# Kernel optimization log

Hardware: AMD Instinct MI355X
Metric: run time of the kernel (lower is better)

The kernel has to match this reference:

```python
import jax, jax.numpy as jnp
import numpy as np

LN_EPS = 1e-3  # keras LayerNormalization default epsilon


def _prefix_weights(S, dtype):
    # W[i, j] = 1/(i-j)^2 for j < i, else 0  (distance = i - j)
    idx = jnp.arange(S)
    diff = idx[:, None] - idx[None, :]
    safe = jnp.where(diff > 0, diff, 1).astype(dtype)
    return jnp.where(diff > 0, 1.0 / (safe * safe), jnp.zeros((), dtype))


def setup_inputs() -> dict:
    key = jax.random.key(0)
    k1, k2 = jax.random.split(key)
    B, S, E = 2, 512, 256
    x = jax.random.normal(k1, (B, S, E), dtype=jnp.float32)
    concept_map = jax.random.normal(k2, (E, E, E), dtype=jnp.float32) * 0.02
    gamma = jnp.ones((E,), dtype=jnp.float32)
    beta = jnp.zeros((E,), dtype=jnp.float32)
    return {"x": x, "concept_map": concept_map, "gamma": gamma, "beta": beta}


def reference(x, concept_map, gamma, beta):
    B, S, E = x.shape
    # positional-weighted prefix sum: s[b,i,:] = sum_{j<i} x[b,j,:] / (i-j)^2
    W = _prefix_weights(S, x.dtype)            # (S, S) lower-triangular
    s = jnp.einsum('ij,bjd->bid', W, x)        # (B, S, E)
    # outer product x_i (x) s_i contracted with cubic concept_map:
    # result[b,i,c] = sum_{a,p} x[b,i,a] * s[b,i,p] * concept_map[c,a,p]
    # (stacked conceptual_matrices broadcast against concept_map, summed over
    #  the last two axes -- equivalent bilinear contraction)
    y = jnp.einsum('bsa,bsp,cap->bsc', x, s, concept_map)
    y = y + x  # residual
    # LayerNormalization over last axis (keras defaults: eps=1e-3, affine)
    mean = jnp.mean(y, axis=-1, keepdims=True)
    var = jnp.mean(jnp.square(y - mean), axis=-1, keepdims=True)
    y = (y - mean) * jax.lax.rsqrt(var + LN_EPS) * gamma + beta
    # Dropout is identity at inference
    return y
```

## Files before the change

### kernel.cpp

```cpp
#include <hip/hip_runtime.h>
#include <hip/hip_fp16.h>
#include <cstdint>

#define BB 2
#define SS 512
#define EE 256
#define NN (BB*SS)
#define KTOT (EE*EE)
#define SPLITK 32
#define KCHUNK (KTOT/SPLITK)
#define NSTEP (KCHUNK/32)
#define TSTEPS (KTOT/32)
#define LN_EPS 1e-3f

typedef _Float16 f16;
typedef _Float16 f16x8 __attribute__((ext_vector_type(8)));
typedef float    f32x4 __attribute__((ext_vector_type(4)));

#define NPACK 512

__global__ void prep_kernel(const float* __restrict__ cm, f16* __restrict__ cmP,
                            const float* __restrict__ x, float* __restrict__ ps) {
    __shared__ __align__(16) char smem[35072];
    const int bid = blockIdx.x;
    const int tid = threadIdx.x;
    const int wave = tid >> 6;
    const int lane = tid & 63;

    if (bid < NPACK) {
        const int cg = bid >> 7;
        const int kg = bid & 127;
        f16* lt = (f16*)smem;
        #pragma unroll
        for (int h = 0; h < 2; ++h) {
            #pragma unroll
            for (int i = 0; i < 8; ++i) {
                const int rl = i * 4 + wave;
                const int row = cg * 64 + h * 32 + rl;
                const float* src = cm + (size_t)row * KTOT + kg * 512 + lane * 8;
                float4 lo = *(const float4*)(src);
                float4 hi = *(const float4*)(src + 4);
                f16x8 v = { (f16)lo.x, (f16)lo.y, (f16)lo.z, (f16)lo.w,
                            (f16)hi.x, (f16)hi.y, (f16)hi.z, (f16)hi.w };
                *(f16x8*)(lt + lane * 264 + rl * 8) = v;
            }
            __syncthreads();
            #pragma unroll
            for (int jj = 0; jj < 8; ++jj) {
                const int s  = jj * 8 + wave * 2 + (lane >> 5);
                const int cl = lane & 31;
                f16x8 v = *(const f16x8*)(lt + s * 264 + cl * 8);
                const int t    = kg * 16 + (s >> 2);
                const int koct = s & 3;
                const int c    = cg * 64 + h * 32 + cl;
                *(f16x8*)(cmP + (size_t)t * 8192 + koct * 2048 + c * 8) = v;
            }
            __syncthreads();
        }
        return;
    }

    float (*xt)[128] = (float(*)[128])smem;
    float* wl2 = (float*)(smem + 32768);
    const int id = bid - NPACK;
    const int eh = id & 1;
    const int rest = id >> 1;
    const int b = rest / 36;
    const int r = rest % 36;
    int it = 0;
    while ((it + 1) * (it + 2) / 2 <= r) ++it;
    const int jt = r - it * (it + 1) / 2;

    for (int t = tid; t < 576; t += 256) {
        const int d = t - 64;
        wl2[t] = (d > 0) ? 1.0f / ((float)d * (float)d) : 0.0f;
    }
    const int jbase = jt * 64, ibase = it * 64;
    const float* xb = x + ((size_t)b * SS + jbase) * EE + eh * 128;
    #pragma unroll
    for (int p = 0; p < 8; ++p) {
        const int row = p * 8 + (tid >> 5);
        const int col = (tid & 31) * 4;
        *(float4*)&xt[row][col] = *(const float4*)(xb + (size_t)row * EE + col);
    }
    __syncthreads();

    const int g  = tid >> 5;
    const int ec = (tid & 31) * 4;
    const int irow = ibase + g * 8;
    float4 acc[8];
    #pragma unroll
    for (int m = 0; m < 8; ++m) acc[m] = (float4){0.f, 0.f, 0.f, 0.f};

    for (int jj = 0; jj < 64; ++jj) {
        const float4 xv = *(const float4*)&xt[jj][ec];
        const int wbase = irow - (jbase + jj) + 64;
        #pragma unroll
        for (int m = 0; m < 8; ++m) {
            const float w = wl2[wbase + m];
            acc[m].x += xv.x * w;
            acc[m].y += xv.y * w;
            acc[m].z += xv.z * w;
            acc[m].w += xv.w * w;
        }
    }

    float* base = ps + ((size_t)(((b * 2 + eh) * 8 + it) * 8 + jt)) * (64 * 128);
    #pragma unroll
    for (int m = 0; m < 8; ++m)
        *(float4*)(base + (size_t)(g * 8 + m) * 128 + ec) = acc[m];
}

__global__ void reduce_s_kernel(const float* __restrict__ ps, float* __restrict__ s) {
    const int n = blockIdx.x;
    const int e = threadIdx.x;
    const int b = n >> 9, i = n & (SS - 1);
    const int it = i >> 6, il = i & 63;
    const int eh = e >> 7, ec = e & 127;
    const size_t tbase = (size_t)((b * 2 + eh) * 8 + it) * 8;
    float acc = 0.0f;
    for (int jt = 0; jt <= it; ++jt)
        acc += ps[(tbase + jt) * (64 * 128) + (size_t)il * 128 + ec];
    s[(size_t)n * EE + e] = acc;
}

__launch_bounds__(256, 2)
__global__ void gemm_kernel(const float* __restrict__ x,
                            const float* __restrict__ sbuf,
                            const f16* __restrict__ cmP,
                            f16* __restrict__ part) {
    __shared__ __align__(16) f16 Bs[4][8192];
    const int tid  = threadIdx.x;
    const int lane = tid & 63;
    const int wave = tid >> 6;
    const int koct = lane >> 4;
    const int cl   = lane & 15;

    const int d = blockIdx.x;
    const int nblock = (d >> 3) & 15;
    const int chunk  = (d & 7) * 4 + (d >> 7);

    f16x8 xf[4];
    #pragma unroll
    for (int rt = 0; rt < 4; ++rt) {
        const int r = nblock * 64 + rt * 16 + cl;
        const float* xr = x + (size_t)r * EE + chunk * 8;
        float4 xlo = *(const float4*)(xr);
        float4 xhi = *(const float4*)(xr + 4);
        xf[rt] = (f16x8){ (f16)xlo.x, (f16)xlo.y, (f16)xlo.z, (f16)xlo.w,
                          (f16)xhi.x, (f16)xhi.y, (f16)xhi.z, (f16)xhi.w };
    }
    float4 p0[4][2];
    #pragma unroll
    for (int rt = 0; rt < 4; ++rt) {
        const int r = nblock * 64 + rt * 16 + cl;
        const float* sr = sbuf + (size_t)r * EE + koct * 8;
        p0[rt][0] = *(const float4*)(sr);
        p0[rt][1] = *(const float4*)(sr + 4);
    }
    __builtin_amdgcn_sched_barrier(0);

    f32x4 acc[4][4];
    #pragma unroll
    for (int a = 0; a < 4; ++a)
        #pragma unroll
        for (int b = 0; b < 4; ++b) acc[a][b] = (f32x4){0.f, 0.f, 0.f, 0.f};

    const char* srcBase = (const char*)cmP + (size_t)(chunk * NSTEP) * 16384;
    auto stageV = [&](int v) {
        const int t = ((v & 7) << 3) | (v >> 3);
        const char* g = srcBase + (size_t)t * 16384 + wave * 1024 + lane * 16;
        char* l = (char*)&Bs[v & 3][0] + wave * 1024;
        #pragma unroll
        for (int i = 0; i < 4; ++i) {
            __builtin_amdgcn_global_load_lds(
                (const __attribute__((address_space(1))) void*)(g + i * 4096),
                (__attribute__((address_space(3))) void*)(l + i * 4096),
                16, 0, 0);
        }
    };

    stageV(0); stageV(1); stageV(2);
    asm volatile("s_waitcnt vmcnt(8)" ::: "memory");
    __builtin_amdgcn_sched_barrier(0);

    f16x8 svm[4];
    #pragma unroll
    for (int rt = 0; rt < 4; ++rt)
        svm[rt] = (f16x8){ (f16)p0[rt][0].x, (f16)p0[rt][0].y,
                           (f16)p0[rt][0].z, (f16)p0[rt][0].w,
                           (f16)p0[rt][1].x, (f16)p0[rt][1].y,
                           (f16)p0[rt][1].z, (f16)p0[rt][1].w };

    const int cb = koct * 2048 + (wave * 64 + cl) * 8;

    f16x8 bfc[4], afc[4];
    {
        const f16* bb = &Bs[0][cb];
        #pragma unroll
        for (int ct = 0; ct < 4; ++ct) bfc[ct] = *(const f16x8*)(bb + ct * 128);
        #pragma unroll
        for (int rt = 0; rt < 4; ++rt) {
            const f16 xa = xf[rt][0];
            const f16x8 xa8 = { xa, xa, xa, xa, xa, xa, xa, xa };
            afc[rt] = xa8 * svm[rt];
        }
    }

    #pragma unroll
    for (int m = 0; m < 8; ++m) {
        float4 pnxt[4][2];
        #pragma unroll
        for (int a_l = 0; a_l < 8; ++a_l) {
            const int v = m * 8 + a_l;

            if (a_l == 6 && m < 7) {
                #pragma unroll
                for (int rt = 0; rt < 4; ++rt) {
                    const int r = nblock * 64 + rt * 16 + cl;
                    const float* sr = sbuf + (size_t)r * EE + (m + 1) * 32 + koct * 8;
                    pnxt[rt][0] = *(const float4*)(sr);
                    pnxt[rt][1] = *(const float4*)(sr + 4);
                }
                __builtin_amdgcn_sched_barrier(0);
            }

            __builtin_amdgcn_s_setprio(1);
            #pragma unroll
            for (int ct = 0; ct < 4; ++ct)
                #pragma unroll
                for (int rt = 0; rt < 4; ++rt)
                    acc[rt][ct] = __builtin_amdgcn_mfma_f32_16x16x32_f16(afc[rt], bfc[ct], acc[rt][ct], 0, 0, 0);
            __builtin_amdgcn_s_setprio(0);

            if (v + 3 < NSTEP) stageV(v + 3);

            if (v <= 60) {
                if (a_l == 6 && m < 7) asm volatile("s_waitcnt vmcnt(16)" ::: "memory");
                else                   asm volatile("s_waitcnt vmcnt(8)"  ::: "memory");
            } else if (v == 61)        asm volatile("s_waitcnt vmcnt(4)"  ::: "memory");
            else if (v == 62)          asm volatile("s_waitcnt vmcnt(0)"  ::: "memory");
            __builtin_amdgcn_sched_barrier(0);

            if (v < 63) {
                const f16* bb = &Bs[0][0] + (size_t)((v + 1) & 3) * 8192 + cb;
                f16x8 bfn[4];
                #pragma unroll
                for (int ct = 0; ct < 4; ++ct) bfn[ct] = *(const f16x8*)(bb + ct * 128);
                if (a_l == 7) {
                    #pragma unroll
                    for (int rt = 0; rt < 4; ++rt)
                        svm[rt] = (f16x8){ (f16)pnxt[rt][0].x, (f16)pnxt[rt][0].y,
                                           (f16)pnxt[rt][0].z, (f16)pnxt[rt][0].w,
                                           (f16)pnxt[rt][1].x, (f16)pnxt[rt][1].y,
                                           (f16)pnxt[rt][1].z, (f16)pnxt[rt][1].w };
                }
                #pragma unroll
                for (int rt = 0; rt < 4; ++rt) {
                    const f16 xa = xf[rt][(a_l + 1) & 7];
                    const f16x8 xa8 = { xa, xa, xa, xa, xa, xa, xa, xa };
                    afc[rt] = xa8 * svm[rt];
                }
                #pragma unroll
                for (int ct = 0; ct < 4; ++ct) bfc[ct] = bfn[ct];
                __builtin_amdgcn_sched_barrier(0);
            }
        }
    }

    __syncthreads();
    f16* Ep = (f16*)&Bs[0][0];
    #pragma unroll
    for (int rt = 0; rt < 4; ++rt) {
        #pragma unroll
        for (int ct = 0; ct < 4; ++ct) {
            const int col = wave * 64 + ct * 16 + cl;
            #pragma unroll
            for (int q = 0; q < 4; ++q) {
                const int lr = rt * 16 + koct * 4 + q;
                Ep[lr * 264 + col] = (f16)acc[rt][ct][q];
            }
        }
    }
    __syncthreads();
    {
        const int lr  = tid >> 2;
        const int seg = tid & 3;
        f16* dst = part + ((size_t)chunk * NN + nblock * 64 + lr) * EE + seg * 64;
        const f16* srcE = Ep + lr * 264 + seg * 64;
        #pragma unroll
        for (int i = 0; i < 8; ++i)
            *(f16x8*)(dst + i * 8) = *(const f16x8*)(srcE + i * 8);
    }
}

__global__ void reduce_ln_kernel(const float* __restrict__ x,
                                 const f16* __restrict__ part,
                                 const float* __restrict__ gamma,
                                 const float* __restrict__ beta,
                                 float* __restrict__ out) {
    const int n = blockIdx.x;
    const int c = threadIdx.x;
    const int lane = c & 63, wave = c >> 6;
    float y = x[(size_t)n * EE + c];
    #pragma unroll 8
    for (int ch = 0; ch < SPLITK; ++ch)
        y += (float)part[((size_t)ch * NN + n) * EE + c];

    float v = y;
    #pragma unroll
    for (int o = 32; o > 0; o >>= 1) v += __shfl_xor(v, o);
    __shared__ float red[8];
    if (lane == 0) red[wave] = v;
    __syncthreads();
    const float mean = (red[0] + red[1] + red[2] + red[3]) * (1.0f / EE);
    const float d = y - mean;
    float sq = d * d;
    #pragma unroll
    for (int o = 32; o > 0; o >>= 1) sq += __shfl_xor(sq, o);
    if (lane == 0) red[4 + wave] = sq;
    __syncthreads();
    const float var = (red[4] + red[5] + red[6] + red[7]) * (1.0f / EE);
    out[(size_t)n * EE + c] = d * rsqrtf(var + LN_EPS) * gamma[c] + beta[c];
}

extern "C" void kernel_launch(void* const* d_in, const int* in_sizes, int n_in,
                              void* d_out, int out_size, void* d_ws, size_t ws_size,
                              hipStream_t stream) {
    const float* x     = (const float*)d_in[0];
    const float* cm    = (const float*)d_in[1];
    const float* gamma = (const float*)d_in[2];
    const float* beta  = (const float*)d_in[3];
    float* out = (float*)d_out;

    float* sbuf = (float*)d_ws;
    f16*   cmP  = (f16*)(sbuf + (size_t)NN * EE);
    f16*   part = (f16*)((char*)cmP + (size_t)TSTEPS * 8192 * sizeof(f16));
    float* ps   = (float*)part;

    hipLaunchKernelGGL(prep_kernel, dim3(NPACK + 144), dim3(256), 0, stream,
                       cm, cmP, x, ps);
    hipLaunchKernelGGL(reduce_s_kernel, dim3(NN), dim3(256), 0, stream, ps, sbuf);
    hipLaunchKernelGGL(gemm_kernel, dim3(16 * SPLITK), dim3(256), 0, stream,
                       x, sbuf, cmP, part);
    hipLaunchKernelGGL(reduce_ln_kernel, dim3(NN), dim3(256), 0, stream,
                       x, part, gamma, beta, out);
}
```

Measured before the change: 75.19 us.

## Switch gemm B staging to double-buffered 2-tile stages with full waits

```diff
diff --git a/kernel.cpp b/kernel.cpp
--- a/kernel.cpp
+++ b/kernel.cpp
@@ -9,7 +9,7 @@
 #define KTOT (EE*EE)
 #define SPLITK 32
 #define KCHUNK (KTOT/SPLITK)
-#define NSTEP (KCHUNK/32)
+#define NSTEP 32
 #define TSTEPS (KTOT/32)
 #define LN_EPS 1e-3f
 
@@ -129,7 +129,7 @@
                             const float* __restrict__ sbuf,
                             const f16* __restrict__ cmP,
                             f16* __restrict__ part) {
-    __shared__ __align__(16) f16 Bs[4][8192];
+    __shared__ __align__(16) f16 Bs[2][16384];
     const int tid  = threadIdx.x;
     const int lane = tid & 63;
     const int wave = tid >> 6;
@@ -166,22 +166,24 @@
         #pragma unroll
         for (int b = 0; b < 4; ++b) acc[a][b] = (f32x4){0.f, 0.f, 0.f, 0.f};
 
-    const char* srcBase = (const char*)cmP + (size_t)(chunk * NSTEP) * 16384;
+    const char* srcBase = (const char*)cmP + (size_t)chunk * 64 * 16384;
     auto stageV = [&](int v) {
-        const int t = ((v & 7) << 3) | (v >> 3);
-        const char* g = srcBase + (size_t)t * 16384 + wave * 1024 + lane * 16;
-        char* l = (char*)&Bs[v & 3][0] + wave * 1024;
-        #pragma unroll
-        for (int i = 0; i < 4; ++i) {
-            __builtin_amdgcn_global_load_lds(
-                (const __attribute__((address_space(1))) void*)(g + i * 4096),
-                (__attribute__((address_space(3))) void*)(l + i * 4096),
-                16, 0, 0);
-        }
+        const int t0 = 16 * (v & 3) + (v >> 2);
+        const char* g = srcBase + (size_t)t0 * 16384 + wave * 1024 + lane * 16;
+        char* l = (char*)&Bs[v & 1][0] + wave * 1024;
+        #pragma unroll
+        for (int tt = 0; tt < 2; ++tt)
+            #pragma unroll
+            for (int i = 0; i < 4; ++i) {
+                __builtin_amdgcn_global_load_lds(
+                    (const __attribute__((address_space(1))) void*)(g + tt * 131072 + i * 4096),
+                    (__attribute__((address_space(3))) void*)(l + tt * 16384 + i * 4096),
+                    16, 0, 0);
+            }
     };
 
-    stageV(0); stageV(1); stageV(2);
-    asm volatile("s_waitcnt vmcnt(8)" ::: "memory");
+    stageV(0);
+    asm volatile("s_waitcnt vmcnt(0)" ::: "memory");
     __builtin_amdgcn_sched_barrier(0);
 
     f16x8 svm[4];
@@ -194,27 +196,68 @@
 
     const int cb = koct * 2048 + (wave * 64 + cl) * 8;
 
-    f16x8 bfc[4], afc[4];
-    {
-        const f16* bb = &Bs[0][cb];
-        #pragma unroll
-        for (int ct = 0; ct < 4; ++ct) bfc[ct] = *(const f16x8*)(bb + ct * 128);
-        #pragma unroll
-        for (int rt = 0; rt < 4; ++rt) {
-            const f16 xa = xf[rt][0];
-            const f16x8 xa8 = { xa, xa, xa, xa, xa, xa, xa, xa };
-            afc[rt] = xa8 * svm[rt];
-        }
-    }
-
     #pragma unroll
     for (int m = 0; m < 8; ++m) {
         float4 pnxt[4][2];
         #pragma unroll
-        for (int a_l = 0; a_l < 8; ++a_l) {
-            const int v = m * 8 + a_l;
-
-            if (a_l == 6 && m < 7) {
+        for (int ap = 0; ap < 4; ++ap) {
+            const int v = m * 4 + ap;
+
+            if (v > 0) {
+                asm volatile("s_waitcnt vmcnt(0)" ::: "memory");
+                __builtin_amdgcn_sched_barrier(0);
+            }
+            if (ap == 0 && m > 0) {
+                #pragma unroll
+                for (int rt = 0; rt < 4; ++rt)
+                    svm[rt] = (f16x8){ (f16)pnxt[rt][0].x, (f16)pnxt[rt][0].y,
+                                       (f16)pnxt[rt][0].z, (f16)pnxt[rt][0].w,
+                                       (f16)pnxt[rt][1].x, (f16)pnxt[rt][1].y,
+                                       (f16)pnxt[rt][1].z, (f16)pnxt[rt][1].w };
+            }
+
+            const f16* bbase = &Bs[v & 1][0];
+
+            f16x8 bf[4];
+            #pragma unroll
+            for (int ct = 0; ct < 4; ++ct)
+                bf[ct] = *(const f16x8*)(bbase + cb + ct * 128);
+
+            if (v + 1 < NSTEP) stageV(v + 1);
+
+            f16x8 af[4];
+            #pragma unroll
+            for (int rt = 0; rt < 4; ++rt) {
+                const f16 xa = xf[rt][2 * ap];
+                const f16x8 xa8 = { xa, xa, xa, xa, xa, xa, xa, xa };
+                af[rt] = xa8 * svm[rt];
+            }
+            __builtin_amdgcn_s_setprio(1);
+            #pragma unroll
+            for (int ct = 0; ct < 4; ++ct)
+                #pragma unroll
+                for (int rt = 0; rt < 4; ++rt)
+                    acc[rt][ct] = __builtin_amdgcn_mfma_f32_16x16x32_f16(af[rt], bf[ct], acc[rt][ct], 0, 0, 0);
+            __builtin_amdgcn_s_setprio(0);
+
+            #pragma unroll
+            for (int ct = 0; ct < 4; ++ct)
+                bf[ct] = *(const f16x8*)(bbase + 8192 + cb + ct * 128);
+            #pragma unroll
+            for (int rt = 0; rt < 4; ++rt) {
+                const f16 xa = xf[rt][2 * ap + 1];
+                const f16x8 xa8 = { xa, xa, xa, xa, xa, xa, xa, xa };
+                af[rt] = xa8 * svm[rt];
+            }
+            __builtin_amdgcn_s_setprio(1);
+            #pragma unroll
+            for (int ct = 0; ct < 4; ++ct)
+                #pragma unroll
+                for (int rt = 0; rt < 4; ++rt)
+                    acc[rt][ct] = __builtin_amdgcn_mfma_f32_16x16x32_f16(af[rt], bf[ct], acc[rt][ct], 0, 0, 0);
+            __builtin_amdgcn_s_setprio(0);
+
+            if (ap == 2 && m < 7) {
                 #pragma unroll
                 for (int rt = 0; rt < 4; ++rt) {
                     const int r = nblock * 64 + rt * 16 + cl;
@@ -222,47 +265,6 @@
                     pnxt[rt][0] = *(const float4*)(sr);
                     pnxt[rt][1] = *(const float4*)(sr + 4);
                 }
-                __builtin_amdgcn_sched_barrier(0);
-            }
-
-            __builtin_amdgcn_s_setprio(1);
-            #pragma unroll
-            for (int ct = 0; ct < 4; ++ct)
-                #pragma unroll
-                for (int rt = 0; rt < 4; ++rt)
-                    acc[rt][ct] = __builtin_amdgcn_mfma_f32_16x16x32_f16(afc[rt], bfc[ct], acc[rt][ct], 0, 0, 0);
-            __builtin_amdgcn_s_setprio(0);
-
-            if (v + 3 < NSTEP) stageV(v + 3);
-
-            if (v <= 60) {
-                if (a_l == 6 && m < 7) asm volatile("s_waitcnt vmcnt(16)" ::: "memory");
-                else                   asm volatile("s_waitcnt vmcnt(8)"  ::: "memory");
-            } else if (v == 61)        asm volatile("s_waitcnt vmcnt(4)"  ::: "memory");
-            else if (v == 62)          asm volatile("s_waitcnt vmcnt(0)"  ::: "memory");
-            __builtin_amdgcn_sched_barrier(0);
-
-            if (v < 63) {
-                const f16* bb = &Bs[0][0] + (size_t)((v + 1) & 3) * 8192 + cb;
-                f16x8 bfn[4];
-                #pragma unroll
-                for (int ct = 0; ct < 4; ++ct) bfn[ct] = *(const f16x8*)(bb + ct * 128);
-                if (a_l == 7) {
-                    #pragma unroll
-                    for (int rt = 0; rt < 4; ++rt)
-                        svm[rt] = (f16x8){ (f16)pnxt[rt][0].x, (f16)pnxt[rt][0].y,
-                                           (f16)pnxt[rt][0].z, (f16)pnxt[rt][0].w,
-                                           (f16)pnxt[rt][1].x, (f16)pnxt[rt][1].y,
-                                           (f16)pnxt[rt][1].z, (f16)pnxt[rt][1].w };
-                }
-                #pragma unroll
-                for (int rt = 0; rt < 4; ++rt) {
-                    const f16 xa = xf[rt][(a_l + 1) & 7];
-                    const f16x8 xa8 = { xa, xa, xa, xa, xa, xa, xa, xa };
-                    afc[rt] = xa8 * svm[rt];
-                }
-                #pragma unroll
-                for (int ct = 0; ct < 4; ++ct) bfc[ct] = bfn[ct];
                 __builtin_amdgcn_sched_barrier(0);
             }
         }
```

After: 79.66 us. +5.9%, slower.

## Load concept-map B fragments directly into registers instead of staging through LDS

Applied to the files above, without the earlier changes.

```diff
diff --git a/kernel.cpp b/kernel.cpp
--- a/kernel.cpp
+++ b/kernel.cpp
@@ -129,7 +129,7 @@
                             const float* __restrict__ sbuf,
                             const f16* __restrict__ cmP,
                             f16* __restrict__ part) {
-    __shared__ __align__(16) f16 Bs[4][8192];
+    __shared__ __align__(16) f16 Ep[64 * 264];
     const int tid  = threadIdx.x;
     const int lane = tid & 63;
     const int wave = tid >> 6;
@@ -158,6 +158,18 @@
         p0[rt][0] = *(const float4*)(sr);
         p0[rt][1] = *(const float4*)(sr + 4);
     }
+
+    const char* bbase = (const char*)cmP + (size_t)chunk * (64 * 16384)
+                      + koct * 4096 + wave * 1024 + cl * 16;
+    #define TOFF(v) ((size_t)((((v) & 7) << 3) | ((v) >> 3)) * 16384)
+    #define LOADB(BUF, v) do {                                              \
+        _Pragma("unroll")                                                   \
+        for (int ct_ = 0; ct_ < 4; ++ct_)                                   \
+            BUF[ct_] = *(const f16x8*)(bbase + TOFF(v) + ct_ * 256);        \
+    } while (0)
+
+    f16x8 b0[4], b1[4], b2[4], b3[4];
+    LOADB(b0, 0); LOADB(b1, 1); LOADB(b2, 2);
     __builtin_amdgcn_sched_barrier(0);
 
     f32x4 acc[4][4];
@@ -165,24 +177,6 @@
     for (int a = 0; a < 4; ++a)
         #pragma unroll
         for (int b = 0; b < 4; ++b) acc[a][b] = (f32x4){0.f, 0.f, 0.f, 0.f};
-
-    const char* srcBase = (const char*)cmP + (size_t)(chunk * NSTEP) * 16384;
-    auto stageV = [&](int v) {
-        const int t = ((v & 7) << 3) | (v >> 3);
-        const char* g = srcBase + (size_t)t * 16384 + wave * 1024 + lane * 16;
-        char* l = (char*)&Bs[v & 3][0] + wave * 1024;
-        #pragma unroll
-        for (int i = 0; i < 4; ++i) {
-            __builtin_amdgcn_global_load_lds(
-                (const __attribute__((address_space(1))) void*)(g + i * 4096),
-                (__attribute__((address_space(3))) void*)(l + i * 4096),
-                16, 0, 0);
-        }
-    };
-
-    stageV(0); stageV(1); stageV(2);
-    asm volatile("s_waitcnt vmcnt(8)" ::: "memory");
-    __builtin_amdgcn_sched_barrier(0);
 
     f16x8 svm[4];
     #pragma unroll
@@ -192,84 +186,64 @@
                            (f16)p0[rt][1].x, (f16)p0[rt][1].y,
                            (f16)p0[rt][1].z, (f16)p0[rt][1].w };
 
-    const int cb = koct * 2048 + (wave * 64 + cl) * 8;
-
-    f16x8 bfc[4], afc[4];
-    {
-        const f16* bb = &Bs[0][cb];
-        #pragma unroll
-        for (int ct = 0; ct < 4; ++ct) bfc[ct] = *(const f16x8*)(bb + ct * 128);
-        #pragma unroll
-        for (int rt = 0; rt < 4; ++rt) {
-            const f16 xa = xf[rt][0];
-            const f16x8 xa8 = { xa, xa, xa, xa, xa, xa, xa, xa };
-            afc[rt] = xa8 * svm[rt];
-        }
-    }
+    float4 pnxt[4][2];
+
+    #define STEP(mm, aa, BU, BL) do {                                       \
+        const int v_ = (mm) * 8 + (aa);                                     \
+        if ((aa) == 6 && (mm) < 7) {                                        \
+            _Pragma("unroll")                                               \
+            for (int rt_ = 0; rt_ < 4; ++rt_) {                             \
+                const int r_ = nblock * 64 + rt_ * 16 + cl;                 \
+                const float* sr_ = sbuf + (size_t)r_ * EE + ((mm) + 1) * 32 \
+                                 + koct * 8;                                \
+                pnxt[rt_][0] = *(const float4*)(sr_);                       \
+                pnxt[rt_][1] = *(const float4*)(sr_ + 4);                   \
+            }                                                               \
+        }                                                                   \
+        f16x8 af_[4];                                                       \
+        _Pragma("unroll")                                                   \
+        for (int rt_ = 0; rt_ < 4; ++rt_) {                                 \
+            const f16 xa_ = xf[rt_][(aa)];                                  \
+            const f16x8 xa8_ = { xa_, xa_, xa_, xa_, xa_, xa_, xa_, xa_ };  \
+            af_[rt_] = xa8_ * svm[rt_];                                     \
+        }                                                                   \
+        __builtin_amdgcn_s_setprio(1);                                      \
+        _Pragma("unroll")                                                   \
+        for (int ct_ = 0; ct_ < 4; ++ct_)                                   \
+            _Pragma("unroll")                                               \
+            for (int rt_ = 0; rt_ < 4; ++rt_)                               \
+                acc[rt_][ct_] = __builtin_amdgcn_mfma_f32_16x16x32_f16(     \
+                    af_[rt_], BU[ct_], acc[rt_][ct_], 0, 0, 0);             \
+        __builtin_amdgcn_s_setprio(0);                                      \
+        if (v_ + 3 < NSTEP) LOADB(BL, v_ + 3);                              \
+        if ((aa) == 7 && (mm) < 7) {                                        \
+            _Pragma("unroll")                                               \
+            for (int rt_ = 0; rt_ < 4; ++rt_)                               \
+                svm[rt_] = (f16x8){                                         \
+                    (f16)pnxt[rt_][0].x, (f16)pnxt[rt_][0].y,               \
+                    (f16)pnxt[rt_][0].z, (f16)pnxt[rt_][0].w,               \
+                    (f16)pnxt[rt_][1].x, (f16)pnxt[rt_][1].y,               \
+                    (f16)pnxt[rt_][1].z, (f16)pnxt[rt_][1].w };             \
+        }                                                                   \
+        __builtin_amdgcn_sched_barrier(0);                                  \
+    } while (0)
 
     #pragma unroll
     for (int m = 0; m < 8; ++m) {
-        float4 pnxt[4][2];
-        #pragma unroll
-        for (int a_l = 0; a_l < 8; ++a_l) {
-            const int v = m * 8 + a_l;
-
-            if (a_l == 6 && m < 7) {
-                #pragma unroll
-                for (int rt = 0; rt < 4; ++rt) {
-                    const int r = nblock * 64 + rt * 16 + cl;
-                    const float* sr = sbuf + (size_t)r * EE + (m + 1) * 32 + koct * 8;
-                    pnxt[rt][0] = *(const float4*)(sr);
-                    pnxt[rt][1] = *(const float4*)(sr + 4);
-                }
-                __builtin_amdgcn_sched_barrier(0);
-            }
-
-            __builtin_amdgcn_s_setprio(1);
-            #pragma unroll
-            for (int ct = 0; ct < 4; ++ct)
-                #pragma unroll
-                for (int rt = 0; rt < 4; ++rt)
-                    acc[rt][ct] = __builtin_amdgcn_mfma_f32_16x16x32_f16(afc[rt], bfc[ct], acc[rt][ct], 0, 0, 0);
-            __builtin_amdgcn_s_setprio(0);
-
-            if (v + 3 < NSTEP) stageV(v + 3);
-
-            if (v <= 60) {
-                if (a_l == 6 && m < 7) asm volatile("s_waitcnt vmcnt(16)" ::: "memory");
-                else                   asm volatile("s_waitcnt vmcnt(8)"  ::: "memory");
-            } else if (v == 61)        asm volatile("s_waitcnt vmcnt(4)"  ::: "memory");
-            else if (v == 62)          asm volatile("s_waitcnt vmcnt(0)"  ::: "memory");
-            __builtin_amdgcn_sched_barrier(0);
-
-            if (v < 63) {
-                const f16* bb = &Bs[0][0] + (size_t)((v + 1) & 3) * 8192 + cb;
-                f16x8 bfn[4];
-                #pragma unroll
-                for (int ct = 0; ct < 4; ++ct) bfn[ct] = *(const f16x8*)(bb + ct * 128);
-                if (a_l == 7) {
-                    #pragma unroll
-                    for (int rt = 0; rt < 4; ++rt)
-                        svm[rt] = (f16x8){ (f16)pnxt[rt][0].x, (f16)pnxt[rt][0].y,
-                                           (f16)pnxt[rt][0].z, (f16)pnxt[rt][0].w,
-                                           (f16)pnxt[rt][1].x, (f16)pnxt[rt][1].y,
-                                           (f16)pnxt[rt][1].z, (f16)pnxt[rt][1].w };
-                }
-                #pragma unroll
-                for (int rt = 0; rt < 4; ++rt) {
-                    const f16 xa = xf[rt][(a_l + 1) & 7];
-                    const f16x8 xa8 = { xa, xa, xa, xa, xa, xa, xa, xa };
-                    afc[rt] = xa8 * svm[rt];
-                }
-                #pragma unroll
-                for (int ct = 0; ct < 4; ++ct) bfc[ct] = bfn[ct];
-                __builtin_amdgcn_sched_barrier(0);
-            }
-        }
-    }
-
-    __syncthreads();
-    f16* Ep = (f16*)&Bs[0][0];
+        STEP(m, 0, b0, b3);
+        STEP(m, 1, b1, b0);
+        STEP(m, 2, b2, b1);
+        STEP(m, 3, b3, b2);
+        STEP(m, 4, b0, b3);
+        STEP(m, 5, b1, b0);
+        STEP(m, 6, b2, b1);
+        STEP(m, 7, b3, b2);
+    }
+    #undef STEP
+    #undef LOADB
+    #undef TOFF
+
+    __syncthreads();
     #pragma unroll
     for (int rt = 0; rt < 4; ++rt) {
         #pragma unroll
```

Measured after the change: 72.34 us. 1.04x faster.
